# Optimization experiments

Measured on AMD Instinct MI355X. Metric: run time of the kernel, lower is better.

## Reference

```python
import jax, jax.numpy as jnp
import numpy as np

B, T = 256, 100
EMBED = 36
DM = 72          # d_model = 2*embed_size
H, E = 4, 18     # n_heads, head dim
PATCH, STRIDE = 16, 8
SEQ = T + 1      # 101
PN = (SEQ - PATCH) // STRIDE + 2  # 12
DFF = 4 * H * DM                  # 1152
EPS = 1e-4

def _pe(periods, freqs):
    i = jnp.arange(periods + 1, dtype=jnp.float32)[:, None]
    j = jnp.arange(freqs, dtype=jnp.float32)[None, :]
    ang = (np.pi / periods) * (2.0 ** j) * (i - 1.0)
    return jnp.concatenate([jnp.sin(ang), jnp.cos(ang)], axis=1)  # [periods+1, 2*freqs]

def _ln(x, g, b):
    m = x.mean(-1, keepdims=True)
    v = ((x - m) ** 2).mean(-1, keepdims=True)
    return (x - m) / jnp.sqrt(v + 1e-5) * g + b

def _masked_stats(x, mask):
    # mean/std (population) over masked entries per row; 0 when mask empty
    cnt = mask.sum(1, keepdims=True).astype(x.dtype)
    safe = jnp.maximum(cnt, 1.0)
    mean = jnp.where(mask, x, 0.0).sum(1, keepdims=True) / safe
    var = jnp.where(mask, (x - mean) ** 2, 0.0).sum(1, keepdims=True) / safe
    nz = cnt > 0
    return jnp.where(nz, mean, 0.0), jnp.where(nz, jnp.sqrt(var), 0.0)

def _fwd(history, w_nopos, b_nopos, w_wpos, b_wpos, task_emb,
         w_inp, b_inp, wq, bq, wk, bk, wv, bv, wo, bo,
         w_ff1, b_ff1, w_ff2, b_ff2, g1, be1, g2, be2, ge, bee,
         w_outp, b_outp, w_head, b_head, ts, target_ts, task):
    pe_year, pe_month, pe_day, pe_dow = _pe(10, 4), _pe(12, 4), _pe(31, 6), _pe(7, 4)
    yr = ts[:, :, 0]
    dy = jnp.clip(yr[:, -1:] - yr, 0, 10)
    pos = jnp.concatenate([pe_year[dy], pe_month[ts[:, :, 1]], pe_day[ts[:, :, 2]], pe_dow[ts[:, :, 3]]], -1)  # [B,T,36]
    # --- RobustScaler, fully vectorized over batch ---
    x = history                                  # [B,T]
    mean, std = _masked_stats(x, x != 0)
    clipped = jnp.clip(x, 0.0, mean + 2.0 * std)
    mc, sc = _masked_stats(clipped, clipped != 0)
    s = mc + sc + EPS                            # [B,1]
    scale = s[:, :, None]                        # [B,1,1]
    h = jnp.clip(x / s, 0.0, 3.0)[..., None]     # [B,T,1]
    # --- embeddings ---
    e0 = jax.nn.relu(h @ w_nopos + b_nopos)
    e1 = jax.nn.relu(h @ w_wpos + b_wpos) + pos
    hist = jnp.concatenate([e0, e1], -1)         # [B,T,72]
    tt = target_ts.reshape(-1, 1, 5)
    yrq = jnp.clip(yr[:, -1:] - tt[:, :, 0], 0, 10)
    qp = jnp.concatenate([pe_year[yrq], pe_month[tt[:, :, 1]], pe_day[tt[:, :, 2]], pe_dow[tt[:, :, 3]]], -1)[:, 0]
    t = task_emb[task]                           # [B,36]
    tgt = jnp.concatenate([t, t + qp], -1)       # [B,72]
    hist = jnp.concatenate([hist, tgt[:, None, :]], 1)  # [B,101,72]
    # --- PAttnBlock ---
    m = jax.lax.stop_gradient(hist.mean(1, keepdims=True))
    xc = hist - m
    sd = jnp.sqrt(xc.var(1, keepdims=True) + 1e-5)
    xc = (xc / sd).transpose(0, 2, 1)            # [B,72,101]
    xp = jnp.concatenate([xc, jnp.repeat(xc[..., -1:], STRIDE, axis=-1)], -1)  # replication pad -> [B,72,109]
    idx = jnp.arange(PN)[:, None] * STRIDE + jnp.arange(PATCH)[None, :]
    patches = xp[..., idx]                       # [B,72,PN,PATCH]
    z = patches @ w_inp + b_inp                  # [B,72,PN,DM]
    Bd = B * DM
    z = z.reshape(Bd, PN, DM)
    q = (z @ wq + bq).reshape(Bd, PN, H, E)
    k = (z @ wk + bk).reshape(Bd, PN, H, E)
    v = (z @ wv + bv).reshape(Bd, PN, H, E)
    A = jax.nn.softmax(jnp.einsum('blhe,bshe->bhls', q, k) / np.sqrt(E).astype(np.float32), axis=-1)
    o = jnp.einsum('bhls,bshd->blhd', A, v).reshape(Bd, PN, DM)
    z = z + (o @ wo + bo)
    z = _ln(z, g1, be1)
    ff = jax.nn.gelu(z @ w_ff1 + b_ff1, approximate=False) @ w_ff2 + b_ff2
    z = _ln(z + ff, g2, be2)
    z = _ln(z, ge, bee)                          # encoder final norm
    z = z.reshape(B, DM, PN * DM)
    out0 = (z @ w_outp + b_outp).transpose(0, 2, 1)   # [B,1,72]
    y = jax.nn.relu(out0 @ w_head + b_head)[..., 0]   # [B,1]
    y = (y * scale[:, :, 0])[:, 0]                    # [B]
    return y, scale

def setup_inputs() -> dict:
    key = jax.random.key(0)
    ks = jax.random.split(key, 20)
    def n(k, shape, s=0.05):
        return jax.random.normal(k, shape, jnp.float32) * s
    inp = {
        'history': jax.random.uniform(ks[0], (B, T), jnp.float32),
        'w_nopos': n(ks[1], (1, EMBED)), 'b_nopos': jnp.zeros((EMBED,), jnp.float32),
        'w_wpos': n(ks[2], (1, EMBED)), 'b_wpos': jnp.zeros((EMBED,), jnp.float32),
        'task_emb': n(ks[3], (10, EMBED), 1.0),
        'w_inp': n(ks[4], (PATCH, DM)), 'b_inp': jnp.zeros((DM,), jnp.float32),
        'wq': n(ks[5], (DM, DM)), 'bq': jnp.zeros((DM,), jnp.float32),
        'wk': n(ks[6], (DM, DM)), 'bk': jnp.zeros((DM,), jnp.float32),
        'wv': n(ks[7], (DM, DM)), 'bv': jnp.zeros((DM,), jnp.float32),
        'wo': n(ks[8], (DM, DM)), 'bo': jnp.zeros((DM,), jnp.float32),
        'w_ff1': n(ks[9], (DM, DFF)), 'b_ff1': jnp.zeros((DFF,), jnp.float32),
        'w_ff2': n(ks[10], (DFF, DM)), 'b_ff2': jnp.zeros((DM,), jnp.float32),
        'g1': jnp.ones((DM,), jnp.float32), 'be1': jnp.zeros((DM,), jnp.float32),
        'g2': jnp.ones((DM,), jnp.float32), 'be2': jnp.zeros((DM,), jnp.float32),
        'ge': jnp.ones((DM,), jnp.float32), 'bee': jnp.zeros((DM,), jnp.float32),
        'w_outp': n(ks[11], (PN * DM, 1)), 'b_outp': jnp.zeros((1,), jnp.float32),
        'w_head': n(ks[12], (DM, 1)), 'b_head': jnp.zeros((1,), jnp.float32),
        'ts': jax.random.randint(ks[13], (B, T, 4), 0, 8),
        'target_ts': jax.random.randint(ks[14], (B, 5), 0, 8),
        'task': jax.random.randint(ks[15], (B,), 0, 10),
    }
    return inp

def reference(history, w_nopos, b_nopos, w_wpos, b_wpos, task_emb,
              w_inp, b_inp, wq, bq, wk, bk, wv, bv, wo, bo,
              w_ff1, b_ff1, w_ff2, b_ff2, g1, be1, g2, be2, ge, bee,
              w_outp, b_outp, w_head, b_head, ts, target_ts, task):
    return _fwd(history, w_nopos, b_nopos, w_wpos, b_wpos, task_emb,
                w_inp, b_inp, wq, bq, wk, bk, wv, bv, wo, bo,
                w_ff1, b_ff1, w_ff2, b_ff2, g1, be1, g2, be2, ge, bee,
                w_outp, b_outp, w_head, b_head, ts, target_ts, task)
```

## Files before the change

kernel.cpp:

```cpp
#include <hip/hip_runtime.h>
#include <hip/hip_bf16.h>

#define B_ 256
#define T_ 100
#define EMBED_ 36
#define DM_ 72
#define H_ 4
#define E_ 18
#define PATCH_ 16
#define STRIDE_ 8
#define SEQ_ 101
#define PN_ 12
#define DFF_ 1152

#define KP 96

#define VT2_OFF 18432
#define PT2_OFF 28224
#define OL2_OFF 30528

typedef __attribute__((ext_vector_type(8))) short s8v;
typedef __attribute__((ext_vector_type(4))) float f32x4;

__device__ __forceinline__ unsigned short f2b(float x) {
  __hip_bfloat16 b = __float2bfloat16(x);
  return __builtin_bit_cast(unsigned short, b);
}
__device__ __forceinline__ unsigned short f2bc(float x) {
  return (unsigned short)((__builtin_bit_cast(unsigned int, x) + 0x8000u) >> 16);
}
__device__ __forceinline__ unsigned int pk2f(float lo, float hi) {
  unsigned int ul = __builtin_bit_cast(unsigned int, lo) + 0x8000u;
  unsigned int uh = __builtin_bit_cast(unsigned int, hi) + 0x8000u;
  return __builtin_amdgcn_perm(uh, ul, 0x07060302u);
}
__device__ __forceinline__ s8v zfrag_global(const float* __restrict__ row, int k0) {
  if (k0 >= 72) {
    uint4 z = {0u, 0u, 0u, 0u};
    if (k0 == 72) z.x = 0x3F80u;
    return __builtin_bit_cast(s8v, z);
  }
  float4 f0 = *(const float4*)(row + k0);
  float4 f1 = *(const float4*)(row + k0 + 4);
  uint4 u;
  u.x = pk2f(f0.x, f0.y); u.y = pk2f(f0.z, f0.w);
  u.z = pk2f(f1.x, f1.y); u.w = pk2f(f1.z, f1.w);
  return __builtin_bit_cast(s8v, u);
}

__device__ __forceinline__ float fast_gelu(float x) {
  float u = x * __builtin_fmaf(0.1029437f, x * x, 2.3022085f);
  float e = exp2f(-u);
  return x * __builtin_amdgcn_rcpf(1.0f + e);
}


__device__ __forceinline__ float block_sum1k(float v, float* redw, float* bcast) {
  const int tid = threadIdx.x;
  #pragma unroll
  for (int m = 32; m > 0; m >>= 1) v += __shfl_xor(v, m, 64);
  if ((tid & 63) == 0) redw[tid >> 6] = v;
  __syncthreads();
  if (tid < 16) {
    float r = redw[tid];
    #pragma unroll
    for (int m = 8; m > 0; m >>= 1) r += __shfl_xor(r, m, 64);
    if (tid == 0) *bcast = r;
  }
  __syncthreads();
  float out = *bcast;
  __syncthreads();
  return out;
}

__device__ __forceinline__ float pe_val(float periods, int freqs, int idx, int c) {
  int f = (c < freqs) ? c : (c - freqs);
  float ang = 3.14159265358979323846f / periods * exp2f((float)f) * ((float)idx - 1.0f);
  return (c < freqs) ? sinf(ang) : cosf(ang);
}

__device__ __forceinline__ float pos_feat(int jj, int dy, int mo, int da, int dw) {
  if (jj < 8)  return pe_val(10.f, 4, dy, jj);
  if (jj < 16) return pe_val(12.f, 4, mo, jj - 8);
  if (jj < 28) return pe_val(31.f, 6, da, jj - 16);
  return pe_val(7.f, 4, dw, jj - 28);
}

__global__ __launch_bounds__(256) void wconv_kernel(
    const float* __restrict__ wq, const float* __restrict__ wk,
    const float* __restrict__ wvp, const float* __restrict__ wo,
    const float* __restrict__ w1, const float* __restrict__ w2,
    const float* __restrict__ bq, const float* __restrict__ bk,
    const float* __restrict__ bv, const float* __restrict__ bo,
    const float* __restrict__ b1,
    unsigned short* __restrict__ wqkvT, unsigned short* __restrict__ woT,
    unsigned short* __restrict__ w1T, unsigned short* __restrict__ w2P)
{
  const float s18 = 0.23570226039551584f;
  int idx = blockIdx.x * 256 + threadIdx.x;
  if (idx < 23040) {
    int n = idx / 96, k = idx % 96;
    int mat = n / 80, nc = n % 80;
    const float* w = (mat == 0) ? wq : (mat == 1) ? wk : wvp;
    const float* bb = (mat == 0) ? bq : (mat == 1) ? bk : bv;
    float scale = (mat == 0) ? s18 : 1.0f;
    unsigned short v = 0;
    if (nc < 72) {
      if (k < 72) v = f2b(w[k * 72 + nc] * scale);
      else if (k == 72) v = f2b(bb[nc] * scale);
    }
    wqkvT[idx] = v;
  } else if (idx < 30720) {
    int i = idx - 23040;
    int n = i / 96, k = i % 96;
    unsigned short v = 0;
    if (n < 72) {
      if (k < 72) v = f2b(wo[k * 72 + n]);
      else if (k == 72) v = f2b(bo[n]);
    }
    woT[i] = v;
  } else if (idx < 141312) {
    int i = idx - 30720;
    int n = i / 96, k = i % 96;
    unsigned short v = 0;
    if (k < 72) v = f2b(w1[(size_t)k * DFF_ + n]);
    else if (k == 72) v = f2b(b1[n]);
    w1T[i] = v;
  } else if (idx < 233472) {
    int i = idx - 141312;
    int slot = i & 7;
    int lane = (i >> 3) & 63;
    int c    = (i >> 9) % 36;
    int mt5  = i / 18432;
    int la = lane & 15, lg = lane >> 4;
    int kl = (slot < 4) ? (4 * lg + slot) : (16 + 4 * lg + (slot - 4));
    int dff = c * 32 + kl;
    int j = mt5 * 16 + la;
    w2P[i] = (j < 72) ? f2b(w2[(size_t)dff * 72 + j]) : (unsigned short)0;
  }
}

__global__ __launch_bounds__(1024) void prep_kernel(
    const float* __restrict__ history,
    const float* __restrict__ w_nopos, const float* __restrict__ b_nopos,
    const float* __restrict__ w_wpos, const float* __restrict__ b_wpos,
    const float* __restrict__ task_emb,
    const float* __restrict__ w_inp, const float* __restrict__ b_inp,
    const int* __restrict__ ts, const int* __restrict__ target_ts,
    const int* __restrict__ task,
    float* __restrict__ zbuf, float* __restrict__ sbuf, float* __restrict__ d_out)
{
  const int b = blockIdx.x, tid = threadIdx.x;
  __shared__ float hs[SEQ_][73];
  __shared__ float redw[16];
  __shared__ float bcast;
  __shared__ float ps1[8][73], ps2[8][73];
  __shared__ float mu[DM_], rsd[DM_];

  const float* x = history + (size_t)b * T_;

  float xv = (tid < T_) ? x[tid] : 0.0f;
  bool msk1 = (tid < T_) && (xv != 0.0f);
  float sum1 = block_sum1k(msk1 ? xv : 0.0f, redw, &bcast);
  float cnt1 = block_sum1k(msk1 ? 1.0f : 0.0f, redw, &bcast);
  float safe1 = fmaxf(cnt1, 1.0f);
  float mean1 = sum1 / safe1;
  float var1 = block_sum1k(msk1 ? (xv - mean1) * (xv - mean1) : 0.0f, redw, &bcast) / safe1;
  float std1 = (cnt1 > 0.f) ? sqrtf(var1) : 0.0f;
  float mn1  = (cnt1 > 0.f) ? mean1 : 0.0f;
  float hi = mn1 + 2.0f * std1;
  float cl = (tid < T_) ? fminf(fmaxf(xv, 0.0f), hi) : 0.0f;

  bool msk2 = (tid < T_) && (cl != 0.0f);
  float sum2 = block_sum1k(msk2 ? cl : 0.0f, redw, &bcast);
  float cnt2 = block_sum1k(msk2 ? 1.0f : 0.0f, redw, &bcast);
  float safe2 = fmaxf(cnt2, 1.0f);
  float mean2 = sum2 / safe2;
  float var2 = block_sum1k(msk2 ? (cl - mean2) * (cl - mean2) : 0.0f, redw, &bcast) / safe2;
  float std2 = (cnt2 > 0.f) ? sqrtf(var2) : 0.0f;
  float mn2  = (cnt2 > 0.f) ? mean2 : 0.0f;
  const float s = mn2 + std2 + 1e-4f;
  if (tid == 0) { sbuf[b] = s; d_out[B_ + b] = s; }

  const int yr_last = ts[((size_t)b * T_ + (T_ - 1)) * 4 + 0];

  for (int o = tid; o < T_ * DM_; o += 1024) {
    int t = o / DM_, j = o % DM_;
    float h = fminf(fmaxf(x[t] / s, 0.0f), 3.0f);
    float val;
    if (j < EMBED_) {
      val = fmaxf(h * w_nopos[j] + b_nopos[j], 0.0f);
    } else {
      int jj = j - EMBED_;
      float e1 = fmaxf(h * w_wpos[jj] + b_wpos[jj], 0.0f);
      const int* tr = ts + ((size_t)b * T_ + t) * 4;
      int dy = min(max(yr_last - tr[0], 0), 10);
      val = e1 + pos_feat(jj, dy, tr[1], tr[2], tr[3]);
    }
    hs[t][j] = val;
  }
  if (tid < DM_) {
    int j = tid;
    float te = task_emb[task[b] * EMBED_ + (j < EMBED_ ? j : j - EMBED_)];
    if (j < EMBED_) {
      hs[T_][j] = te;
    } else {
      int jj = j - EMBED_;
      const int* qr = target_ts + (size_t)b * 5;
      int yq = min(max(yr_last - qr[0], 0), 10);
      hs[T_][j] = te + pos_feat(jj, yq, qr[1], qr[2], qr[3]);
    }
  }
  __syncthreads();

  if (tid < 576) {
    int d = tid % 72, c = tid / 72;
    int t0 = c * 13, t1 = min(t0 + 13, SEQ_);
    float a1 = 0.f, a2 = 0.f;
    for (int t = t0; t < t1; t++) { float v = hs[t][d]; a1 += v; a2 += v * v; }
    ps1[c][d] = a1; ps2[c][d] = a2;
  }
  __syncthreads();
  if (tid < DM_) {
    float S1 = 0.f, S2 = 0.f;
    #pragma unroll
    for (int c = 0; c < 8; c++) { S1 += ps1[c][tid]; S2 += ps2[c][tid]; }
    float m = S1 * (1.0f / (float)SEQ_);
    float v = fmaxf(S2 * (1.0f / (float)SEQ_) - m * m, 0.f);
    mu[tid] = m; rsd[tid] = rsqrtf(v + 1e-5f);
  }
  __syncthreads();
  for (int o = tid; o < SEQ_ * DM_; o += 1024) {
    int t = o / DM_, d = o % DM_;
    hs[t][d] = (hs[t][d] - mu[d]) * rsd[d];
  }
  __syncthreads();

  for (int o4 = tid; o4 < DM_ * PN_ * (DM_ / 4); o4 += 1024) {
    int jg = o4 % 18, p = (o4 / 18) % PN_, d = o4 / (18 * PN_);
    float4 acc = *(const float4*)&b_inp[jg * 4];
    #pragma unroll
    for (int i = 0; i < PATCH_; i++) {
      int t = p * STRIDE_ + i;
      if (t > T_) t = T_;
      float hv = hs[t][d];
      float4 w4 = *(const float4*)&w_inp[i * DM_ + jg * 4];
      acc.x += hv * w4.x; acc.y += hv * w4.y; acc.z += hv * w4.z; acc.w += hv * w4.w;
    }
    *(float4*)&zbuf[((size_t)(b * DM_ + d) * PN_ + p) * DM_ + jg * 4] = acc;
  }
}

__global__ __launch_bounds__(384) void attn_kernel(
    const unsigned short* __restrict__ wqkvT, const unsigned short* __restrict__ woT,
    const float* __restrict__ g1, const float* __restrict__ be1,
    float* __restrict__ zf)
{
  __shared__ __attribute__((aligned(16))) unsigned short AS[38288];

  const int tid = threadIdx.x;
  const int lane = tid & 63, wid = tid >> 6;
  const int m0 = wid * 16;
  const int la = lane & 15, lg = lane >> 4;
  float* zg = zf + (size_t)blockIdx.x * 8 * PN_ * DM_;

  const f32x4 Z4 = {0.f, 0.f, 0.f, 0.f};
  const uint4 ZU = {0u, 0u, 0u, 0u};
  const s8v ZF = __builtin_bit_cast(s8v, ZU);

  for (int i = tid; i < 768; i += 384) {
    int bofs = i * 24 + 18;
    *(unsigned int*)&AS[bofs] = 0u; *(unsigned int*)&AS[bofs + 2] = 0u;
    *(unsigned int*)&AS[bofs + 4] = 0u;
  }
  for (int i = tid; i < 576; i += 384) {
    int h = i / 144, rem = i % 144, e = rem / 8, r = rem % 8;
    int bofs = VT2_OFF + h * 2448 + e * 136 + r * 16 + 12;
    *(unsigned int*)&AS[bofs] = 0u; *(unsigned int*)&AS[bofs + 2] = 0u;
  }
  for (int i = tid; i < 72; i += 384) {
    int bofs = VT2_OFF + (i / 18) * 2448 + (i % 18) * 136 + 128;
    *(unsigned int*)&AS[bofs] = 0u; *(unsigned int*)&AS[bofs + 2] = 0u;
    *(unsigned int*)&AS[bofs + 4] = 0u; *(unsigned int*)&AS[bofs + 6] = 0u;
  }
  for (int i = tid; i < 1152; i += 384)
    ((unsigned int*)&AS[PT2_OFF])[i] = 0u;
  for (int i = tid; i < 96; i += 384) {
    int bofs = OL2_OFF + i * 80 + 72;
    *(unsigned int*)&AS[bofs] = 0x3F80u;
    *(unsigned int*)&AS[bofs + 2] = 0u; *(unsigned int*)&AS[bofs + 4] = 0u;
    *(unsigned int*)&AS[bofs + 6] = 0u;
  }
  for (int i = tid; i < 40; i += 384)
    ((unsigned int*)&AS[OL2_OFF + 96 * 80])[i] = 0u;

  {
    s8v A[3];
    #pragma unroll
    for (int kc = 0; kc < 3; kc++)
      A[kc] = zfrag_global(zg + (m0 + la) * 72, kc * 32 + 8 * lg);

    for (int n0 = 0; n0 < 15; n0++) {
      const int ng = n0 * 16 + la;
      const int mat = ng / 80, nc = ng % 80;
      const int hh = nc / 18, ee = nc % 18;
      f32x4 acc = Z4;
      #pragma unroll
      for (int kc = 0; kc < 3; kc++) {
        s8v Bf = *(const s8v*)&wqkvT[(size_t)ng * KP + kc * 32 + 8 * lg];
        acc = __builtin_amdgcn_mfma_f32_16x16x32_bf16(A[kc], Bf, acc, 0, 0, 0);
      }
      if (nc < 72) {
        if (mat < 2) {
          const int base = ((mat * 4 + hh) * 96) * 24 + ee;
          #pragma unroll
          for (int r = 0; r < 4; r++)
            AS[base + (m0 + 4 * lg + r) * 24] = f2bc(acc[r]);
        } else {
          const int basev = VT2_OFF + hh * 2448 + ee * 136;
          #pragma unroll
          for (int r = 0; r < 4; r++) {
            int tok = m0 + 4 * lg + r;
            AS[basev + (tok / 12) * 16 + tok % 12] = f2bc(acc[r]);
          }
        }
      }
    }
  }
  __syncthreads();

  {
    const float LOG2E = 1.4426950408889634f;
    const int ptb = PT2_OFF + wid * 384;
    for (int u = wid; u < 32; u += 6) {
      const int rg = u >> 2, h = u & 3;
      const int tokb = rg * 12;
      s8v Aq = *(const s8v*)&AS[((0 * 4 + h) * 96 + tokb + la) * 24 + 8 * lg];
      s8v Bk = *(const s8v*)&AS[((1 * 4 + h) * 96 + tokb + la) * 24 + 8 * lg];
      if (lg == 3) { Aq = ZF; Bk = ZF; }
      f32x4 S = __builtin_amdgcn_mfma_f32_16x16x32_bf16(Aq, Bk, Z4, 0, 0, 0);

      float p[4], rcs[4];
      #pragma unroll
      for (int rr = 0; rr < 4; rr++) {
        float t = (la < 12) ? S[rr] : -3.0e38f;
        float mx = t;
        mx = fmaxf(mx, __shfl_xor(mx, 1, 64));
        mx = fmaxf(mx, __shfl_xor(mx, 2, 64));
        mx = fmaxf(mx, __shfl_xor(mx, 4, 64));
        mx = fmaxf(mx, __shfl_xor(mx, 8, 64));
        float pe = exp2f((t - mx) * LOG2E);
        float sm = pe;
        sm += __shfl_xor(sm, 1, 64);
        sm += __shfl_xor(sm, 2, 64);
        sm += __shfl_xor(sm, 4, 64);
        sm += __shfl_xor(sm, 8, 64);
        p[rr] = pe;
        rcs[rr] = __builtin_amdgcn_rcpf(sm);
      }
      #pragma unroll
      for (int rr = 0; rr < 4; rr++)
        AS[ptb + (4 * lg + rr) * 24 + la] = f2bc(p[rr] * rcs[rr]);

      s8v Ap = *(const s8v*)&AS[ptb + la * 24 + 8 * lg];
      if (lg == 3) Ap = ZF;
      s8v Bv0 = *(const s8v*)&AS[VT2_OFF + h * 2448 + la * 136 + rg * 16 + 8 * lg];
      f32x4 O0 = __builtin_amdgcn_mfma_f32_16x16x32_bf16(Ap, Bv0, Z4, 0, 0, 0);
      s8v Bv1 = *(const s8v*)&AS[VT2_OFF + h * 2448 + (16 + la) * 136 + rg * 16 + 8 * lg];
      f32x4 O1 = __builtin_amdgcn_mfma_f32_16x16x32_bf16(Ap, Bv1, Z4, 0, 0, 0);

      if (lg < 3) {
        #pragma unroll
        for (int rr = 0; rr < 4; rr++) {
          int l = 4 * lg + rr;
          AS[OL2_OFF + (tokb + l) * 80 + h * 18 + la] = f2bc(O0[rr]);
          if (la < 2)
            AS[OL2_OFF + (tokb + l) * 80 + h * 18 + 16 + la] = f2bc(O1[rr]);
        }
      }
    }
  }
  __syncthreads();

  {
    s8v A[3];
    #pragma unroll
    for (int kc = 0; kc < 3; kc++)
      A[kc] = *(const s8v*)&AS[OL2_OFF + (m0 + la) * 80 + kc * 32 + 8 * lg];

    f32x4 acc[5];
    #pragma unroll
    for (int n0 = 0; n0 < 5; n0++) {
      acc[n0] = Z4;
      #pragma unroll
      for (int kc = 0; kc < 3; kc++) {
        s8v Bf = *(const s8v*)&woT[(size_t)(n0 * 16 + la) * KP + kc * 32 + 8 * lg];
        acc[n0] = __builtin_amdgcn_mfma_f32_16x16x32_bf16(A[kc], Bf, acc[n0], 0, 0, 0);
      }
    }

    const float inv72 = 1.0f / 72.0f;
    float g1v[5], be1v[5];
    #pragma unroll
    for (int n0 = 0; n0 < 5; n0++) {
      bool ok = (n0 < 4) || (la < 8);
      g1v[n0]  = ok ? g1[n0 * 16 + la] : 0.f;
      be1v[n0] = ok ? be1[n0 * 16 + la] : 0.f;
    }
    #pragma unroll
    for (int r = 0; r < 4; r++) {
      const int t = m0 + 4 * lg + r;
      float vals[5];
      float s1 = 0.f, s2 = 0.f;
      #pragma unroll
      for (int n0 = 0; n0 < 5; n0++) {
        bool ok = (n0 < 4) || (la < 8);
        float x = ok ? (acc[n0][r] + zg[t * 72 + n0 * 16 + la]) : 0.f;
        vals[n0] = x; s1 += x; s2 += x * x;
      }
      s1 += __shfl_xor(s1, 1, 64); s1 += __shfl_xor(s1, 2, 64);
      s1 += __shfl_xor(s1, 4, 64); s1 += __shfl_xor(s1, 8, 64);
      s2 += __shfl_xor(s2, 1, 64); s2 += __shfl_xor(s2, 2, 64);
      s2 += __shfl_xor(s2, 4, 64); s2 += __shfl_xor(s2, 8, 64);
      float mean = s1 * inv72;
      float rs = rsqrtf(fmaxf(s2 * inv72 - mean * mean, 0.f) + 1e-5f);
      #pragma unroll
      for (int n0 = 0; n0 < 5; n0++)
        if ((n0 < 4) || (la < 8))
          zg[t * 72 + n0 * 16 + la] = (vals[n0] - mean) * rs * g1v[n0] + be1v[n0];
    }
  }
}

__global__ __launch_bounds__(128) void ff_kernel(
    const unsigned short* __restrict__ w1T, const unsigned short* __restrict__ w2P,
    const float* __restrict__ b2,
    const float* __restrict__ g2p, const float* __restrict__ be2,
    const float* __restrict__ gep, const float* __restrict__ beep,
    float* __restrict__ zf)
{
  const int tid = threadIdx.x;
  const int lane = tid & 63, wid = tid >> 6;
  const int la = lane & 15, lg = lane >> 4;
  const int tb = wid * 48;
  float* zg = zf + (size_t)blockIdx.x * 96 * DM_;

  const f32x4 Z4 = {0.f, 0.f, 0.f, 0.f};

  s8v Z[3][3];
  #pragma unroll
  for (int nt = 0; nt < 3; nt++)
    #pragma unroll
    for (int kc = 0; kc < 3; kc++)
      Z[nt][kc] = zfrag_global(zg + (tb + nt * 16 + la) * 72, kc * 32 + 8 * lg);

  f32x4 acc2[5][3];
  #pragma unroll
  for (int mt = 0; mt < 5; mt++) {
    f32x4 binit = Z4;
    if (mt < 4 || lg < 2) {
      float bb[4];
      *(float4*)bb = *(const float4*)&b2[mt * 16 + 4 * lg];
      binit[0] = bb[0]; binit[1] = bb[1]; binit[2] = bb[2]; binit[3] = bb[3];
    }
    #pragma unroll
    for (int nt = 0; nt < 3; nt++) acc2[mt][nt] = binit;
  }

  const int w1l = la * 96 + 8 * lg;
  const int w2l = lane * 8;

  s8v Af[6], A2r[5];
  #pragma unroll
  for (int mt = 0; mt < 2; mt++)
    #pragma unroll
    for (int kc = 0; kc < 3; kc++)
      Af[mt * 3 + kc] = *(const s8v*)&w1T[mt * 1536 + kc * 32 + w1l];
  #pragma unroll
  for (int mt = 0; mt < 5; mt++)
    A2r[mt] = *(const s8v*)&w2P[mt * 18432 + w2l];

  for (int c = 0; c < 36; c++) {
    const int cn = (c + 1 < 36) ? c + 1 : 35;
    const int n3072 = cn * 3072, n512 = cn * 512;

    f32x4 D1[2][3];
    #pragma unroll
    for (int mt = 0; mt < 2; mt++)
      #pragma unroll
      for (int nt = 0; nt < 3; nt++) D1[mt][nt] = Z4;
    #pragma unroll
    for (int mt = 0; mt < 2; mt++)
      #pragma unroll
      for (int kc = 0; kc < 3; kc++)
        #pragma unroll
        for (int nt = 0; nt < 3; nt++)
          D1[mt][nt] = __builtin_amdgcn_mfma_f32_16x16x32_bf16(Af[mt * 3 + kc], Z[nt][kc], D1[mt][nt], 0, 0, 0);

    #pragma unroll
    for (int mt = 0; mt < 2; mt++)
      #pragma unroll
      for (int kc = 0; kc < 3; kc++)
        Af[mt * 3 + kc] = *(const s8v*)&w1T[n3072 + mt * 1536 + kc * 32 + w1l];

    s8v B2[3];
    #pragma unroll
    for (int nt = 0; nt < 3; nt++) {
      uint4 u;
      u.x = pk2f(fast_gelu(D1[0][nt][0]), fast_gelu(D1[0][nt][1]));
      u.y = pk2f(fast_gelu(D1[0][nt][2]), fast_gelu(D1[0][nt][3]));
      u.z = pk2f(fast_gelu(D1[1][nt][0]), fast_gelu(D1[1][nt][1]));
      u.w = pk2f(fast_gelu(D1[1][nt][2]), fast_gelu(D1[1][nt][3]));
      B2[nt] = __builtin_bit_cast(s8v, u);
    }

    #pragma unroll
    for (int mt = 0; mt < 5; mt++)
      #pragma unroll
      for (int nt = 0; nt < 3; nt++)
        acc2[mt][nt] = __builtin_amdgcn_mfma_f32_16x16x32_bf16(A2r[mt], B2[nt], acc2[mt][nt], 0, 0, 0);

    #pragma unroll
    for (int mt = 0; mt < 5; mt++)
      A2r[mt] = *(const s8v*)&w2P[mt * 18432 + n512 + w2l];
  }

  const float inv72 = 1.0f / 72.0f;
  #pragma unroll
  for (int nt = 0; nt < 3; nt++) {
    const int t = tb + nt * 16 + la;
    float v[5][4];
    float s1 = 0.f, s2 = 0.f;
    #pragma unroll
    for (int mt = 0; mt < 5; mt++) {
      if (mt < 4 || lg < 2) {
        float rr[4];
        *(float4*)rr = *(const float4*)&zg[t * 72 + mt * 16 + 4 * lg];
        #pragma unroll
        for (int r = 0; r < 4; r++) {
          float x = acc2[mt][nt][r] + rr[r];
          v[mt][r] = x; s1 += x; s2 += x * x;
        }
      } else {
        #pragma unroll
        for (int r = 0; r < 4; r++) v[mt][r] = 0.f;
      }
    }
    s1 += __shfl_xor(s1, 16, 64); s1 += __shfl_xor(s1, 32, 64);
    s2 += __shfl_xor(s2, 16, 64); s2 += __shfl_xor(s2, 32, 64);
    float mean = s1 * inv72;
    float rs = rsqrtf(fmaxf(s2 * inv72 - mean * mean, 0.f) + 1e-5f);

    float w[5][4];
    float t1 = 0.f, t2 = 0.f;
    #pragma unroll
    for (int mt = 0; mt < 5; mt++) {
      if (mt < 4 || lg < 2) {
        float gg[4], bb[4];
        *(float4*)gg = *(const float4*)&g2p[mt * 16 + 4 * lg];
        *(float4*)bb = *(const float4*)&be2[mt * 16 + 4 * lg];
        #pragma unroll
        for (int r = 0; r < 4; r++) {
          float x = (v[mt][r] - mean) * rs * gg[r] + bb[r];
          w[mt][r] = x; t1 += x; t2 += x * x;
        }
      } else {
        #pragma unroll
        for (int r = 0; r < 4; r++) w[mt][r] = 0.f;
      }
    }
    t1 += __shfl_xor(t1, 16, 64); t1 += __shfl_xor(t1, 32, 64);
    t2 += __shfl_xor(t2, 16, 64); t2 += __shfl_xor(t2, 32, 64);
    float m2 = t1 * inv72;
    float rs2 = rsqrtf(fmaxf(t2 * inv72 - m2 * m2, 0.f) + 1e-5f);

    #pragma unroll
    for (int mt = 0; mt < 5; mt++) {
      if (mt < 4 || lg < 2) {
        float gg[4], bb[4], o[4];
        *(float4*)gg = *(const float4*)&gep[mt * 16 + 4 * lg];
        *(float4*)bb = *(const float4*)&beep[mt * 16 + 4 * lg];
        #pragma unroll
        for (int r = 0; r < 4; r++)
          o[r] = (w[mt][r] - m2) * rs2 * gg[r] + bb[r];
        *(float4*)&zg[t * 72 + mt * 16 + 4 * lg] = *(const float4*)o;
      }
    }
  }
}

__global__ __launch_bounds__(256) void final_kernel(
    const float* __restrict__ zbuf,
    const float* __restrict__ w_outp, const float* __restrict__ b_outp,
    const float* __restrict__ w_head, const float* __restrict__ b_head,
    const float* __restrict__ sbuf, float* __restrict__ d_out)
{
  const int b = blockIdx.x, tid = threadIdx.x;
  const int wave = tid >> 6, lane = tid & 63;
  __shared__ float out0[DM_];
  const float* zb = zbuf + (size_t)b * DM_ * (PN_ * DM_);

  for (int d = wave; d < DM_; d += 4) {
    float acc = 0.f;
    for (int e = lane; e < PN_ * DM_; e += 64) acc += zb[(size_t)d * PN_ * DM_ + e] * w_outp[e];
    #pragma unroll
    for (int m = 32; m > 0; m >>= 1) acc += __shfl_xor(acc, m, 64);
    if (lane == 0) out0[d] = acc + b_outp[0];
  }
  __syncthreads();
  if (tid == 0) {
    float acc = b_head[0];
    for (int d = 0; d < DM_; d++) acc += out0[d] * w_head[d];
    d_out[b] = fmaxf(acc, 0.0f) * sbuf[b];
  }
}

extern "C" void kernel_launch(void* const* d_in, const int* in_sizes, int n_in,
                              void* d_out, int out_size, void* d_ws, size_t ws_size,
                              hipStream_t stream) {
  const float* history  = (const float*)d_in[0];
  const float* w_nopos  = (const float*)d_in[1];
  const float* b_nopos  = (const float*)d_in[2];
  const float* w_wpos   = (const float*)d_in[3];
  const float* b_wpos   = (const float*)d_in[4];
  const float* task_emb = (const float*)d_in[5];
  const float* w_inp    = (const float*)d_in[6];
  const float* b_inp    = (const float*)d_in[7];
  const float* wq = (const float*)d_in[8];
  const float* bq = (const float*)d_in[9];
  const float* wk = (const float*)d_in[10];
  const float* bk = (const float*)d_in[11];
  const float* wv = (const float*)d_in[12];
  const float* bv = (const float*)d_in[13];
  const float* wo = (const float*)d_in[14];
  const float* bo = (const float*)d_in[15];
  const float* w_ff1 = (const float*)d_in[16];
  const float* b_ff1 = (const float*)d_in[17];
  const float* w_ff2 = (const float*)d_in[18];
  const float* b_ff2 = (const float*)d_in[19];
  const float* g1  = (const float*)d_in[20];
  const float* be1 = (const float*)d_in[21];
  const float* g2  = (const float*)d_in[22];
  const float* be2 = (const float*)d_in[23];
  const float* ge  = (const float*)d_in[24];
  const float* bee = (const float*)d_in[25];
  const float* w_outp = (const float*)d_in[26];
  const float* b_outp = (const float*)d_in[27];
  const float* w_head = (const float*)d_in[28];
  const float* b_head = (const float*)d_in[29];
  const int* ts        = (const int*)d_in[30];
  const int* target_ts = (const int*)d_in[31];
  const int* task      = (const int*)d_in[32];

  float* out = (float*)d_out;
  char* ws = (char*)d_ws;
  float* zf   = (float*)ws;
  float* sbuf = (float*)(ws + 63700992);
  unsigned short* wqkvT = (unsigned short*)(ws + 63702016);
  unsigned short* woT   = (unsigned short*)(ws + 63748096);
  unsigned short* w1T   = (unsigned short*)(ws + 63763456);
  unsigned short* w2P   = (unsigned short*)(ws + 63984640);

  wconv_kernel<<<912, 256, 0, stream>>>(wq, wk, wv, wo, w_ff1, w_ff2,
      bq, bk, bv, bo, b_ff1, wqkvT, woT, w1T, w2P);
  prep_kernel<<<B_, 1024, 0, stream>>>(history, w_nopos, b_nopos, w_wpos, b_wpos,
      task_emb, w_inp, b_inp, ts, target_ts, task, zf, sbuf, out);
  attn_kernel<<<2304, 384, 0, stream>>>(wqkvT, woT, g1, be1, zf);
  ff_kernel<<<2304, 128, 0, stream>>>(w1T, w2P, b_ff2, g2, be2, ge, bee, zf);
  final_kernel<<<B_, 256, 0, stream>>>(zf, w_outp, b_outp, w_head, b_head, sbuf, out);
}
```

Before: 443.9 us.

## Fuse attention and feed-forward kernels, keep post-LN1 activations in LDS

```diff
diff --git a/kernel.cpp b/kernel.cpp
--- a/kernel.cpp
+++ b/kernel.cpp
@@ -34,7 +34,7 @@
   unsigned int uh = __builtin_bit_cast(unsigned int, hi) + 0x8000u;
   return __builtin_amdgcn_perm(uh, ul, 0x07060302u);
 }
-__device__ __forceinline__ s8v zfrag_global(const float* __restrict__ row, int k0) {
+__device__ __forceinline__ s8v zfrag_any(const float* row, int k0) {
   if (k0 >= 72) {
     uint4 z = {0u, 0u, 0u, 0u};
     if (k0 == 72) z.x = 0x3F80u;
@@ -251,12 +251,17 @@
   }
 }
 
-__global__ __launch_bounds__(384) void attn_kernel(
+__global__ __launch_bounds__(384) void block_kernel(
     const unsigned short* __restrict__ wqkvT, const unsigned short* __restrict__ woT,
+    const unsigned short* __restrict__ w1T, const unsigned short* __restrict__ w2P,
     const float* __restrict__ g1, const float* __restrict__ be1,
+    const float* __restrict__ b2,
+    const float* __restrict__ g2p, const float* __restrict__ be2,
+    const float* __restrict__ gep, const float* __restrict__ beep,
     float* __restrict__ zf)
 {
   __shared__ __attribute__((aligned(16))) unsigned short AS[38288];
+  float* z1f = (float*)AS;
 
   const int tid = threadIdx.x;
   const int lane = tid & 63, wid = tid >> 6;
@@ -298,7 +303,7 @@
     s8v A[3];
     #pragma unroll
     for (int kc = 0; kc < 3; kc++)
-      A[kc] = zfrag_global(zg + (m0 + la) * 72, kc * 32 + 8 * lg);
+      A[kc] = zfrag_any(zg + (m0 + la) * 72, kc * 32 + 8 * lg);
 
     for (int n0 = 0; n0 < 15; n0++) {
       const int ng = n0 * 16 + la;
@@ -427,118 +432,89 @@
       #pragma unroll
       for (int n0 = 0; n0 < 5; n0++)
         if ((n0 < 4) || (la < 8))
-          zg[t * 72 + n0 * 16 + la] = (vals[n0] - mean) * rs * g1v[n0] + be1v[n0];
-    }
-  }
-}
-
-__global__ __launch_bounds__(128) void ff_kernel(
-    const unsigned short* __restrict__ w1T, const unsigned short* __restrict__ w2P,
-    const float* __restrict__ b2,
-    const float* __restrict__ g2p, const float* __restrict__ be2,
-    const float* __restrict__ gep, const float* __restrict__ beep,
-    float* __restrict__ zf)
-{
-  const int tid = threadIdx.x;
-  const int lane = tid & 63, wid = tid >> 6;
-  const int la = lane & 15, lg = lane >> 4;
-  const int tb = wid * 48;
-  float* zg = zf + (size_t)blockIdx.x * 96 * DM_;
-
-  const f32x4 Z4 = {0.f, 0.f, 0.f, 0.f};
-
-  s8v Z[3][3];
-  #pragma unroll
-  for (int nt = 0; nt < 3; nt++)
+          z1f[t * 76 + n0 * 16 + la] = (vals[n0] - mean) * rs * g1v[n0] + be1v[n0];
+    }
+  }
+  __syncthreads();
+
+  {
+    const int tb2 = wid * 16;
+    s8v Z2[3];
     #pragma unroll
     for (int kc = 0; kc < 3; kc++)
-      Z[nt][kc] = zfrag_global(zg + (tb + nt * 16 + la) * 72, kc * 32 + 8 * lg);
-
-  f32x4 acc2[5][3];
-  #pragma unroll
-  for (int mt = 0; mt < 5; mt++) {
-    f32x4 binit = Z4;
-    if (mt < 4 || lg < 2) {
-      float bb[4];
-      *(float4*)bb = *(const float4*)&b2[mt * 16 + 4 * lg];
-      binit[0] = bb[0]; binit[1] = bb[1]; binit[2] = bb[2]; binit[3] = bb[3];
-    }
-    #pragma unroll
-    for (int nt = 0; nt < 3; nt++) acc2[mt][nt] = binit;
-  }
-
-  const int w1l = la * 96 + 8 * lg;
-  const int w2l = lane * 8;
-
-  s8v Af[6], A2r[5];
-  #pragma unroll
-  for (int mt = 0; mt < 2; mt++)
-    #pragma unroll
-    for (int kc = 0; kc < 3; kc++)
-      Af[mt * 3 + kc] = *(const s8v*)&w1T[mt * 1536 + kc * 32 + w1l];
-  #pragma unroll
-  for (int mt = 0; mt < 5; mt++)
-    A2r[mt] = *(const s8v*)&w2P[mt * 18432 + w2l];
-
-  for (int c = 0; c < 36; c++) {
-    const int cn = (c + 1 < 36) ? c + 1 : 35;
-    const int n3072 = cn * 3072, n512 = cn * 512;
-
-    f32x4 D1[2][3];
+      Z2[kc] = zfrag_any(z1f + (tb2 + la) * 76, kc * 32 + 8 * lg);
+
+    f32x4 acc2[5];
+    #pragma unroll
+    for (int mt = 0; mt < 5; mt++) {
+      f32x4 binit = Z4;
+      if (mt < 4 || lg < 2) {
+        float bb[4];
+        *(float4*)bb = *(const float4*)&b2[mt * 16 + 4 * lg];
+        binit[0] = bb[0]; binit[1] = bb[1]; binit[2] = bb[2]; binit[3] = bb[3];
+      }
+      acc2[mt] = binit;
+    }
+
+    const int w1l = la * 96 + 8 * lg;
+    const int w2l = lane * 8;
+
+    s8v Af[6], A2r[5];
     #pragma unroll
     for (int mt = 0; mt < 2; mt++)
       #pragma unroll
-      for (int nt = 0; nt < 3; nt++) D1[mt][nt] = Z4;
-    #pragma unroll
-    for (int mt = 0; mt < 2; mt++)
-      #pragma unroll
       for (int kc = 0; kc < 3; kc++)
-        #pragma unroll
-        for (int nt = 0; nt < 3; nt++)
-          D1[mt][nt] = __builtin_amdgcn_mfma_f32_16x16x32_bf16(Af[mt * 3 + kc], Z[nt][kc], D1[mt][nt], 0, 0, 0);
-
-    #pragma unroll
-    for (int mt = 0; mt < 2; mt++)
-      #pragma unroll
-      for (int kc = 0; kc < 3; kc++)
-        Af[mt * 3 + kc] = *(const s8v*)&w1T[n3072 + mt * 1536 + kc * 32 + w1l];
-
-    s8v B2[3];
-    #pragma unroll
-    for (int nt = 0; nt < 3; nt++) {
+        Af[mt * 3 + kc] = *(const s8v*)&w1T[mt * 1536 + kc * 32 + w1l];
+    #pragma unroll
+    for (int mt = 0; mt < 5; mt++)
+      A2r[mt] = *(const s8v*)&w2P[mt * 18432 + w2l];
+
+    for (int c = 0; c < 36; c++) {
+      const int cn = (c + 1 < 36) ? c + 1 : 35;
+      const int n3072 = cn * 3072, n512 = cn * 512;
+
+      f32x4 D1[2];
+      D1[0] = Z4; D1[1] = Z4;
+      #pragma unroll
+      for (int mt = 0; mt < 2; mt++)
+        #pragma unroll
+        for (int kc = 0; kc < 3; kc++)
+          D1[mt] = __builtin_amdgcn_mfma_f32_16x16x32_bf16(Af[mt * 3 + kc], Z2[kc], D1[mt], 0, 0, 0);
+
+      #pragma unroll
+      for (int mt = 0; mt < 2; mt++)
+        #pragma unroll
+        for (int kc = 0; kc < 3; kc++)
+          Af[mt * 3 + kc] = *(const s8v*)&w1T[n3072 + mt * 1536 + kc * 32 + w1l];
+
       uint4 u;
-      u.x = pk2f(fast_gelu(D1[0][nt][0]), fast_gelu(D1[0][nt][1]));
-      u.y = pk2f(fast_gelu(D1[0][nt][2]), fast_gelu(D1[0][nt][3]));
-      u.z = pk2f(fast_gelu(D1[1][nt][0]), fast_gelu(D1[1][nt][1]));
-      u.w = pk2f(fast_gelu(D1[1][nt][2]), fast_gelu(D1[1][nt][3]));
-      B2[nt] = __builtin_bit_cast(s8v, u);
-    }
-
-    #pragma unroll
-    for (int mt = 0; mt < 5; mt++)
-      #pragma unroll
-      for (int nt = 0; nt < 3; nt++)
-        acc2[mt][nt] = __builtin_amdgcn_mfma_f32_16x16x32_bf16(A2r[mt], B2[nt], acc2[mt][nt], 0, 0, 0);
-
-    #pragma unroll
-    for (int mt = 0; mt < 5; mt++)
-      A2r[mt] = *(const s8v*)&w2P[mt * 18432 + n512 + w2l];
-  }
-
-  const float inv72 = 1.0f / 72.0f;
-  #pragma unroll
-  for (int nt = 0; nt < 3; nt++) {
-    const int t = tb + nt * 16 + la;
+      u.x = pk2f(fast_gelu(D1[0][0]), fast_gelu(D1[0][1]));
+      u.y = pk2f(fast_gelu(D1[0][2]), fast_gelu(D1[0][3]));
+      u.z = pk2f(fast_gelu(D1[1][0]), fast_gelu(D1[1][1]));
+      u.w = pk2f(fast_gelu(D1[1][2]), fast_gelu(D1[1][3]));
+      s8v B2 = __builtin_bit_cast(s8v, u);
+
+      #pragma unroll
+      for (int mt = 0; mt < 5; mt++)
+        acc2[mt] = __builtin_amdgcn_mfma_f32_16x16x32_bf16(A2r[mt], B2, acc2[mt], 0, 0, 0);
+
+      #pragma unroll
+      for (int mt = 0; mt < 5; mt++)
+        A2r[mt] = *(const s8v*)&w2P[mt * 18432 + n512 + w2l];
+    }
+
+    const float inv72 = 1.0f / 72.0f;
+    const int t = tb2 + la;
     float v[5][4];
     float s1 = 0.f, s2 = 0.f;
     #pragma unroll
     for (int mt = 0; mt < 5; mt++) {
       if (mt < 4 || lg < 2) {
         float rr[4];
-        *(float4*)rr = *(const float4*)&zg[t * 72 + mt * 16 + 4 * lg];
+        *(float4*)rr = *(const float4*)&z1f[t * 76 + mt * 16 + 4 * lg];
         #pragma unroll
         for (int r = 0; r < 4; r++) {
-          float x = acc2[mt][nt][r] + rr[r];
+          float x = acc2[mt][r] + rr[r];
           v[mt][r] = x; s1 += x; s2 += x * x;
         }
       } else {
@@ -589,7 +565,7 @@
   }
 }
 
-__global__ __launch_bounds__(256) void final_kernel(
+__global__ __launch_bounds__(1024) void final_kernel(
     const float* __restrict__ zbuf,
     const float* __restrict__ w_outp, const float* __restrict__ b_outp,
     const float* __restrict__ w_head, const float* __restrict__ b_head,
@@ -600,7 +576,7 @@
   __shared__ float out0[DM_];
   const float* zb = zbuf + (size_t)b * DM_ * (PN_ * DM_);
 
-  for (int d = wave; d < DM_; d += 4) {
+  for (int d = wave; d < DM_; d += 16) {
     float acc = 0.f;
     for (int e = lane; e < PN_ * DM_; e += 64) acc += zb[(size_t)d * PN_ * DM_ + e] * w_outp[e];
     #pragma unroll
@@ -665,7 +641,7 @@
       bq, bk, bv, bo, b_ff1, wqkvT, woT, w1T, w2P);
   prep_kernel<<<B_, 1024, 0, stream>>>(history, w_nopos, b_nopos, w_wpos, b_wpos,
       task_emb, w_inp, b_inp, ts, target_ts, task, zf, sbuf, out);
-  attn_kernel<<<2304, 384, 0, stream>>>(wqkvT, woT, g1, be1, zf);
-  ff_kernel<<<2304, 128, 0, stream>>>(w1T, w2P, b_ff2, g2, be2, ge, bee, zf);
-  final_kernel<<<B_, 256, 0, stream>>>(zf, w_outp, b_outp, w_head, b_head, sbuf, out);
-}
+  block_kernel<<<2304, 384, 0, stream>>>(wqkvT, woT, w1T, w2P, g1, be1,
+      b_ff2, g2, be2, ge, bee, zf);
+  final_kernel<<<B_, 1024, 0, stream>>>(zf, w_outp, b_outp, w_head, b_head, sbuf, out);
+}
```

Result: slower. 464.2 us (+4.6%).
